# Optimization experiments

Measured on AMD Instinct MI355X. Metric: run time of the kernel, lower is better.

The kernel has to match this reference:

```python
import jax, jax.numpy as jnp
import numpy as np

D_MODEL = 1024
N_HEADS = 16
D_HEAD = 64
B, S = 8, 1024
EPS = 1.1920929e-07  # torch.finfo(float32).eps, RMSNorm default eps=None


def setup_inputs() -> dict:
    key = jax.random.key(0)
    k1, k2, k3 = jax.random.split(key, 3)
    x = jax.random.normal(k1, (B, S, D_MODEL), dtype=jnp.float32)
    W_qkv = jax.random.normal(k2, (3 * N_HEADS * D_HEAD, D_MODEL), dtype=jnp.float32) * 0.02
    b_qkv = jnp.zeros((3 * N_HEADS * D_HEAD,), dtype=jnp.float32)
    W_o = jax.random.normal(k3, (D_MODEL, N_HEADS * D_HEAD), dtype=jnp.float32) * 0.02
    b_o = jnp.zeros((D_MODEL,), dtype=jnp.float32)
    return {"x": x, "W_qkv": W_qkv, "b_qkv": b_qkv, "W_o": W_o, "b_o": b_o}


def reference(x, W_qkv, b_qkv, W_o, b_o):
    # RMSNorm, no affine
    normed = x * jax.lax.rsqrt(jnp.mean(x * x, axis=-1, keepdims=True) + EPS)
    qkv = normed @ W_qkv.T + b_qkv                       # [b, s, 3*H*Dh]
    # packing order '(n_heads d_head n_qkv)' -> reshape (H, Dh, 3), unbind last
    qkv = qkv.reshape(*qkv.shape[:-1], N_HEADS, D_HEAD, 3)
    q, k, v = qkv[..., 0], qkv[..., 1], qkv[..., 2]       # [b, s, H, Dh]
    scores = jnp.einsum('bqhd,bkhd->bhqk', q, k)          # no 1/sqrt(d) scaling
    seq = x.shape[-2]
    causal_mask = jnp.triu(jnp.ones((seq, seq), dtype=bool), k=1)  # True above diag
    scores = jnp.where(causal_mask, -jnp.inf, scores)
    # NOTE: softmax over the QUERY axis (dim=-2), faithful to the source
    attn = jax.nn.softmax(scores, axis=-2)                # [b, h, q, k]
    z = jnp.einsum('bhqk,bkhd->bqhd', attn, v)            # [b, q, H, Dh]
    z = z.reshape(*z.shape[:-2], N_HEADS * D_HEAD)
    return z @ W_o.T + b_o
```

## Files before the change

### kernel.cpp

```cpp
#include <hip/hip_runtime.h>
#include <hip/hip_bf16.h>

typedef _Float16 f16;
typedef _Float16 f16x8 __attribute__((ext_vector_type(8)));
typedef _Float16 f16x4 __attribute__((ext_vector_type(4)));
typedef float f32x4 __attribute__((ext_vector_type(4)));

constexpr int Bb = 8, Ss = 1024, Hh = 16, DH = 64, DM = 1024, N3 = 3072;
constexpr int Mm = Bb * Ss;
constexpr float EPS = 1.1920929e-07f;

__device__ __forceinline__ void gll16(const f16* g, f16* l) {
    __builtin_amdgcn_global_load_lds(
        (__attribute__((address_space(1))) void*)(g),
        (__attribute__((address_space(3))) void*)(l), 16, 0, 0);
}

__global__ void prep_kernel(const float* __restrict__ x, f16* __restrict__ xh,
                            const float* __restrict__ Wqkv, const float* __restrict__ Wo,
                            f16* __restrict__ wq, f16* __restrict__ wo) {
    const int t = threadIdx.x;
    const int blk = blockIdx.x;
    if (blk < Mm) {
        const int row = blk;
        float4 v = *(const float4*)(x + (size_t)row * DM + t * 4);
        float s = v.x * v.x + v.y * v.y + v.z * v.z + v.w * v.w;
#pragma unroll
        for (int o = 32; o > 0; o >>= 1) s += __shfl_down(s, o, 64);
        __shared__ float red[4];
        if ((t & 63) == 0) red[t >> 6] = s;
        __syncthreads();
        float tot = red[0] + red[1] + red[2] + red[3];
        float sc = rsqrtf(tot * (1.0f / DM) + EPS);
        f16x4 hv = {(f16)(v.x * sc), (f16)(v.y * sc), (f16)(v.z * sc), (f16)(v.w * sc)};
        *(f16x4*)(xh + (size_t)row * DM + t * 4) = hv;
    } else if (blk < Mm + N3) {
        int j = blk - Mm;
        int h = j / 192, r = j % 192, d = r / 3, wh = r % 3;
        int rp = wh * 1024 + h * 64 + d;
        float4 v = *(const float4*)(Wqkv + (size_t)j * DM + t * 4);
        f16x4 hv = {(f16)v.x, (f16)v.y, (f16)v.z, (f16)v.w};
        *(f16x4*)(wq + (size_t)rp * DM + t * 4) = hv;
    } else {
        int j = blk - Mm - N3;
        float4 v = *(const float4*)(Wo + (size_t)j * DM + t * 4);
        f16x4 hv = {(f16)v.x, (f16)v.y, (f16)v.z, (f16)v.w};
        *(f16x4*)(wo + (size_t)j * DM + t * 4) = hv;
    }
}

__launch_bounds__(256, 2)
__global__ void qkv_gemm(const f16* __restrict__ xh, const f16* __restrict__ wq,
                         const float* __restrict__ bqkv, f16* __restrict__ qk,
                         f16* __restrict__ vT) {
    __shared__ __align__(16) f16 smem[17536];
    f16* As = smem;
    f16* Bs = smem + 8192;
    f16* Cs = smem;
    const int t = threadIdx.x, lane = t & 63, w = t >> 6;
    const int bid = blockIdx.y * gridDim.x + blockIdx.x;
    const int swz = (bid & 7) * 192 + (bid >> 3);
    const int gm0 = (swz / 24) * 128, gn0 = (swz % 24) * 128;
    const int wm = (w >> 1) * 64, wn = (w & 1) * 64;
    const int srow = lane >> 3, sslot = (lane & 7) ^ srow;
    const int r15 = lane & 15, cs = lane >> 4;

    const f16* Ag = xh + (size_t)(gm0 + srow) * DM + sslot * 8;
    const f16* Bg = wq + (size_t)(gn0 + srow) * DM + sslot * 8;

    int aoff[4][2], boff[4][2];
#pragma unroll
    for (int i = 0; i < 4; ++i) {
        int Ra = wm + i * 16 + r15;
        aoff[i][0] = Ra * 64 + ((cs ^ (Ra & 7)) * 8);
        aoff[i][1] = Ra * 64 + (((cs + 4) ^ (Ra & 7)) * 8);
        int Rb = wn + i * 16 + r15;
        boff[i][0] = Rb * 64 + ((cs ^ (Rb & 7)) * 8);
        boff[i][1] = Rb * 64 + (((cs + 4) ^ (Rb & 7)) * 8);
    }
    f32x4 acc[4][4] = {};

    for (int k0 = 0; k0 < DM; k0 += 64) {
        __syncthreads();
#pragma unroll
        for (int j = 0; j < 4; ++j) {
            int c = w * 4 + j;
            gll16(Ag + (size_t)c * 8 * DM + k0, As + c * 512);
            gll16(Bg + (size_t)c * 8 * DM + k0, Bs + c * 512);
        }
        __syncthreads();
#pragma unroll
        for (int half = 0; half < 2; ++half) {
            f16x8 af[4], bf[4];
#pragma unroll
            for (int i = 0; i < 4; ++i) af[i] = *(const f16x8*)&As[aoff[i][half]];
#pragma unroll
            for (int i = 0; i < 4; ++i) bf[i] = *(const f16x8*)&Bs[boff[i][half]];
#pragma unroll
            for (int mi = 0; mi < 4; ++mi)
#pragma unroll
                for (int ni = 0; ni < 4; ++ni)
                    acc[mi][ni] = __builtin_amdgcn_mfma_f32_16x16x32_f16(af[mi], bf[ni], acc[mi][ni], 0, 0, 0);
        }
    }

    const int which = gn0 >> 10;
    const int CSTR = (which == 2) ? 137 : 136;
    __syncthreads();
#pragma unroll
    for (int ni = 0; ni < 4; ++ni) {
        int jcolp = gn0 + wn + ni * 16 + r15;
        int rr = jcolp & 1023, hh = rr >> 6, dd = rr & 63;
        float bb = bqkv[hh * 192 + dd * 3 + which];
#pragma unroll
        for (int mi = 0; mi < 4; ++mi)
#pragma unroll
            for (int jj = 0; jj < 4; ++jj)
                Cs[(wm + mi * 16 + cs * 4 + jj) * CSTR + (wn + ni * 16 + r15)] =
                    (f16)(acc[mi][ni][jj] + bb);
    }
    __syncthreads();
    const int bglob = gm0 >> 10;
    const int sbase = gm0 & 1023;
    if (which < 2) {
        f16* dstb = qk + (size_t)which * (Bb * Hh) * (Ss * DH);
#pragma unroll
        for (int it = 0; it < 8; ++it) {
            int lin = it * 2048 + t * 8;
            int row = lin >> 7, c0 = lin & 127;
            f16x8 v = *(const f16x8*)&Cs[row * 136 + c0];
            int rr = (gn0 + c0) & 1023;
            int hh = rr >> 6, d0 = rr & 63;
            *(f16x8*)(dstb + ((size_t)(bglob * Hh + hh)) * (Ss * DH) +
                      (size_t)(sbase + row) * DH + d0) = v;
        }
    } else {
#pragma unroll
        for (int it = 0; it < 8; ++it) {
            int col = it * 16 + (t >> 4);
            int s0 = (t & 15) * 8;
            f16x8 v;
#pragma unroll
            for (int e = 0; e < 8; ++e) v[e] = Cs[(s0 + e) * 137 + col];
            int rr = (gn0 + col) & 1023;
            int hh = rr >> 6, dd = rr & 63;
            *(f16x8*)(vT + ((size_t)(bglob * Hh + hh) * DH + dd) * Ss + sbase + s0) = v;
        }
    }
}

__launch_bounds__(512, 2)
__global__ void colstats_kernel(const f16* __restrict__ qk, float* __restrict__ cbuf) {
    __shared__ __align__(16) f16 Qs[2][128 * 64];
    const int t = threadIdx.x, lane = t & 63, w = t >> 6;
    const int r15 = lane & 15, cs = lane >> 4;
    const int srow = lane >> 3, sslot = (lane & 7) ^ srow;
    const int bh = blockIdx.y, si = blockIdx.x;
    const int kA0 = si * 128, kB0 = (7 - si) * 128;
    const size_t hs = (size_t)(Bb * Hh) * (Ss * DH);
    const f16* qb = qk + (size_t)bh * (Ss * DH);
    const f16* kb = qb + hs;

    const int kwA = kA0 + w * 16, kglobA = kwA + r15;
    const int kwB = kB0 + w * 16, kglobB = kwB + r15;
    f16x8 kfA0 = *(const f16x8*)(kb + (size_t)(kwA + r15) * DH + cs * 8);
    f16x8 kfA1 = *(const f16x8*)(kb + (size_t)(kwA + r15) * DH + 32 + cs * 8);
    f16x8 kfB0 = *(const f16x8*)(kb + (size_t)(kwB + r15) * DH + cs * 8);
    f16x8 kfB1 = *(const f16x8*)(kb + (size_t)(kwB + r15) * DH + 32 + cs * 8);

    gll16(qb + (size_t)(si * 128 + w * 16 + srow) * DH + sslot * 8, Qs[0] + (2 * w) * 512);
    gll16(qb + (size_t)(si * 128 + w * 16 + 8 + srow) * DH + sslot * 8, Qs[0] + (2 * w + 1) * 512);
    __syncthreads();
    float la = 0.0f, lb = 0.0f;
    int cur = 0;

    for (int qt2 = si; qt2 < 8; ++qt2) {
        if (qt2 + 1 < 8) {
            gll16(qb + (size_t)((qt2 + 1) * 128 + w * 16 + srow) * DH + sslot * 8,
                  Qs[cur ^ 1] + (2 * w) * 512);
            gll16(qb + (size_t)((qt2 + 1) * 128 + w * 16 + 8 + srow) * DH + sslot * 8,
                  Qs[cur ^ 1] + (2 * w + 1) * 512);
        }
#pragma unroll
        for (int qs = 0; qs < 8; ++qs) {
            const int qb16 = qt2 * 128 + qs * 16;
            const bool nA = (qb16 + 15 >= kwA);
            const bool nB = (qb16 + 15 >= kwB);
            if (!(nA || nB)) continue;
            int Ra = qs * 16 + r15;
            f16x8 a0 = *(const f16x8*)&Qs[cur][Ra * 64 + ((cs ^ (Ra & 7)) * 8)];
            f16x8 a1 = *(const f16x8*)&Qs[cur][Ra * 64 + (((cs + 4) ^ (Ra & 7)) * 8)];
            if (nA) {
                f32x4 sf = {};
                sf = __builtin_amdgcn_mfma_f32_16x16x32_f16(a0, kfA0, sf, 0, 0, 0);
                sf = __builtin_amdgcn_mfma_f32_16x16x32_f16(a1, kfA1, sf, 0, 0, 0);
#pragma unroll
                for (int j = 0; j < 4; ++j) {
                    int q = qb16 + cs * 4 + j;
                    la += (q >= kglobA) ? __expf(sf[j]) : 0.0f;
                }
            }
            if (nB) {
                f32x4 sf = {};
                sf = __builtin_amdgcn_mfma_f32_16x16x32_f16(a0, kfB0, sf, 0, 0, 0);
                sf = __builtin_amdgcn_mfma_f32_16x16x32_f16(a1, kfB1, sf, 0, 0, 0);
#pragma unroll
                for (int j = 0; j < 4; ++j) {
                    int q = qb16 + cs * 4 + j;
                    lb += (q >= kglobB) ? __expf(sf[j]) : 0.0f;
                }
            }
        }
        __syncthreads();
        cur ^= 1;
    }
    la += __shfl_xor(la, 16, 64);
    la += __shfl_xor(la, 32, 64);
    lb += __shfl_xor(lb, 16, 64);
    lb += __shfl_xor(lb, 32, 64);
    if (cs == 0) {
        cbuf[bh * Ss + kglobA] = logf(la);
        cbuf[bh * Ss + kglobB] = logf(lb);
    }
}

__launch_bounds__(512, 2)
__global__ void attnz_kernel(const f16* __restrict__ qk, const f16* __restrict__ vT,
                             const float* __restrict__ cbuf, f16* __restrict__ z) {
    __shared__ __align__(16) f16 Ks[64 * 64];
    __shared__ __align__(16) f16 Vs[64 * 64];
    __shared__ __align__(16) float cb[1024];
    const int t = threadIdx.x, lane = t & 63, w = t >> 6;
    const int r15 = lane & 15, cs = lane >> 4;
    const int srow = lane >> 3, sslot = (lane & 7) ^ srow;
    const int bh = blockIdx.y, si = blockIdx.x;
    const int qtA = si, qtB = 7 - si;
    const size_t hs = (size_t)(Bb * Hh) * (Ss * DH);
    const f16* qb = qk + (size_t)bh * (Ss * DH);
    const f16* kb = qb + hs;
    const f16* vb = vT + (size_t)bh * (DH * Ss);

    const int qwA = qtA * 128 + w * 16, qA = qwA + r15;
    const int qwB = qtB * 128 + w * 16, qB = qwB + r15;
    f16x8 aqA0 = *(const f16x8*)(qb + (size_t)(qwA + r15) * DH + cs * 8);
    f16x8 aqA1 = *(const f16x8*)(qb + (size_t)(qwA + r15) * DH + 32 + cs * 8);
    f16x8 aqB0 = *(const f16x8*)(qb + (size_t)(qwB + r15) * DH + cs * 8);
    f16x8 aqB1 = *(const f16x8*)(qb + (size_t)(qwB + r15) * DH + 32 + cs * 8);

    gll16(kb + (size_t)(w * 8 + srow) * DH + sslot * 8, Ks + w * 512);
    gll16(vb + (size_t)(w * 8 + srow) * Ss + sslot * 8, Vs + w * 512);
    {
        float2 c2 = *(const float2*)(cbuf + bh * Ss + t * 2);
        *(float2*)&cb[t * 2] = c2;
    }
    __syncthreads();
    f32x4 accA[4] = {}, accB[4] = {};
    const int nktA = 2 * qtA + 2, nktB = 2 * qtB + 2;
    const int sAl = ((cs & 1) * 2) * 16 + r15;
    const int sBl = sAl + 16;
    const bool hi = (cs >> 1) != 0;

    for (int kt = 0; kt < nktB; ++kt) {
        if (kt) {
            __syncthreads();
            gll16(kb + (size_t)(kt * 64 + w * 8 + srow) * DH + sslot * 8, Ks + w * 512);
            gll16(vb + (size_t)(w * 8 + srow) * Ss + kt * 64 + sslot * 8, Vs + w * 512);
            __syncthreads();
        }
        const int kb0 = kt * 64;
        const bool doA = (kt < nktA) && (kb0 <= qwA + 15);
        const bool doB = (kb0 <= qwB + 15);
        if (!(doA || doB)) continue;

        unsigned pkA[4][2], pkB[4][2];
#pragma unroll
        for (int tl = 0; tl < 4; ++tl) {
            const int kbase = kb0 + tl * 16;
            const bool nA = doA && (kbase <= qwA + 15);
            const bool nB = doB && (kbase <= qwB + 15);
            pkA[tl][0] = 0u; pkA[tl][1] = 0u;
            pkB[tl][0] = 0u; pkB[tl][1] = 0u;
            if (!(nA || nB)) continue;
            int Rk2 = tl * 16 + r15;
            f16x8 kf0 = *(const f16x8*)&Ks[Rk2 * 64 + ((cs ^ (Rk2 & 7)) * 8)];
            f16x8 kf1 = *(const f16x8*)&Ks[Rk2 * 64 + (((cs + 4) ^ (Rk2 & 7)) * 8)];
            f32x4 cv = *(const f32x4*)&cb[kbase + cs * 4];
            if (nA) {
                f32x4 sf = {};
                sf = __builtin_amdgcn_mfma_f32_16x16x32_f16(kf0, aqA0, sf, 0, 0, 0);
                sf = __builtin_amdgcn_mfma_f32_16x16x32_f16(kf1, aqA1, sf, 0, 0, 0);
                f16 p[4];
#pragma unroll
                for (int j = 0; j < 4; ++j) {
                    int k = kbase + cs * 4 + j;
                    p[j] = (f16)((k <= qA) ? __expf(sf[j] - cv[j]) : 0.0f);
                }
                union { f16 h[2]; unsigned u; } u0, u1;
                u0.h[0] = p[0]; u0.h[1] = p[1];
                u1.h[0] = p[2]; u1.h[1] = p[3];
                pkA[tl][0] = u0.u; pkA[tl][1] = u1.u;
            }
            if (nB) {
                f32x4 sf = {};
                sf = __builtin_amdgcn_mfma_f32_16x16x32_f16(kf0, aqB0, sf, 0, 0, 0);
                sf = __builtin_amdgcn_mfma_f32_16x16x32_f16(kf1, aqB1, sf, 0, 0, 0);
                f16 p[4];
#pragma unroll
                for (int j = 0; j < 4; ++j) {
                    int k = kbase + cs * 4 + j;
                    p[j] = (f16)((k <= qB) ? __expf(sf[j] - cv[j]) : 0.0f);
                }
                union { f16 h[2]; unsigned u; } u0, u1;
                u0.h[0] = p[0]; u0.h[1] = p[1];
                u1.h[0] = p[2]; u1.h[1] = p[3];
                pkB[tl][0] = u0.u; pkB[tl][1] = u1.u;
            }
        }
        f16x8 bfA[2], bfB[2];
        bool uA[2], uB[2];
#pragma unroll
        for (int c = 0; c < 2; ++c) {
            uA[c] = doA && (kb0 + c * 32 <= qwA + 15);
            uB[c] = doB && (kb0 + c * 32 <= qwB + 15);
            if (uA[c]) {
                unsigned a0 = (unsigned)__shfl((int)pkA[2 * c][0], sAl, 64);
                unsigned a1 = (unsigned)__shfl((int)pkA[2 * c][1], sAl, 64);
                unsigned a2 = (unsigned)__shfl((int)pkA[2 * c][0], sBl, 64);
                unsigned a3 = (unsigned)__shfl((int)pkA[2 * c][1], sBl, 64);
                unsigned b0_ = (unsigned)__shfl((int)pkA[2 * c + 1][0], sAl, 64);
                unsigned b1_ = (unsigned)__shfl((int)pkA[2 * c + 1][1], sAl, 64);
                unsigned b2_ = (unsigned)__shfl((int)pkA[2 * c + 1][0], sBl, 64);
                unsigned b3_ = (unsigned)__shfl((int)pkA[2 * c + 1][1], sBl, 64);
                union { unsigned u[4]; f16x8 v; } bf;
                bf.u[0] = hi ? b0_ : a0;
                bf.u[1] = hi ? b1_ : a1;
                bf.u[2] = hi ? b2_ : a2;
                bf.u[3] = hi ? b3_ : a3;
                bfA[c] = bf.v;
            }
            if (uB[c]) {
                unsigned a0 = (unsigned)__shfl((int)pkB[2 * c][0], sAl, 64);
                unsigned a1 = (unsigned)__shfl((int)pkB[2 * c][1], sAl, 64);
                unsigned a2 = (unsigned)__shfl((int)pkB[2 * c][0], sBl, 64);
                unsigned a3 = (unsigned)__shfl((int)pkB[2 * c][1], sBl, 64);
                unsigned b0_ = (unsigned)__shfl((int)pkB[2 * c + 1][0], sAl, 64);
                unsigned b1_ = (unsigned)__shfl((int)pkB[2 * c + 1][1], sAl, 64);
                unsigned b2_ = (unsigned)__shfl((int)pkB[2 * c + 1][0], sBl, 64);
                unsigned b3_ = (unsigned)__shfl((int)pkB[2 * c + 1][1], sBl, 64);
                union { unsigned u[4]; f16x8 v; } bf;
                bf.u[0] = hi ? b0_ : a0;
                bf.u[1] = hi ? b1_ : a1;
                bf.u[2] = hi ? b2_ : a2;
                bf.u[3] = hi ? b3_ : a3;
                bfB[c] = bf.v;
            }
        }
#pragma unroll
        for (int dt = 0; dt < 4; ++dt) {
            int Rv = dt * 16 + r15;
            f16x8 v0 = *(const f16x8*)&Vs[Rv * 64 + ((cs ^ (Rv & 7)) * 8)];
            f16x8 v1 = *(const f16x8*)&Vs[Rv * 64 + (((4 + cs) ^ (Rv & 7)) * 8)];
            if (uA[0]) accA[dt] = __builtin_amdgcn_mfma_f32_16x16x32_f16(v0, bfA[0], accA[dt], 0, 0, 0);
            if (uA[1]) accA[dt] = __builtin_amdgcn_mfma_f32_16x16x32_f16(v1, bfA[1], accA[dt], 0, 0, 0);
            if (uB[0]) accB[dt] = __builtin_amdgcn_mfma_f32_16x16x32_f16(v0, bfB[0], accB[dt], 0, 0, 0);
            if (uB[1]) accB[dt] = __builtin_amdgcn_mfma_f32_16x16x32_f16(v1, bfB[1], accB[dt], 0, 0, 0);
        }
    }
    const int b = bh >> 4, h = bh & 15;
#pragma unroll
    for (int dt = 0; dt < 4; ++dt) {
        f16x4 zvA = {(f16)accA[dt][0], (f16)accA[dt][1], (f16)accA[dt][2], (f16)accA[dt][3]};
        *(f16x4*)(z + ((size_t)(b * Ss + qA)) * DM + h * DH + dt * 16 + cs * 4) = zvA;
        f16x4 zvB = {(f16)accB[dt][0], (f16)accB[dt][1], (f16)accB[dt][2], (f16)accB[dt][3]};
        *(f16x4*)(z + ((size_t)(b * Ss + qB)) * DM + h * DH + dt * 16 + cs * 4) = zvB;
    }
}

__launch_bounds__(256, 2)
__global__ void out_gemm(const f16* __restrict__ z, const f16* __restrict__ wo,
                         const float* __restrict__ bo, float* __restrict__ out) {
    __shared__ __align__(16) char smem[128 * 132 * 4];
    f16* As = (f16*)smem;
    f16* Bs = (f16*)(smem + 16384);
    float* Cs = (float*)smem;
    const int t = threadIdx.x, lane = t & 63, w = t >> 6;
    const int bid = blockIdx.y * gridDim.x + blockIdx.x;
    const int swz = (bid & 7) * 64 + (bid >> 3);
    const int gm0 = (swz / 8) * 128, gn0 = (swz % 8) * 128;
    const int wm = (w >> 1) * 64, wn = (w & 1) * 64;
    const int srow = lane >> 3, sslot = (lane & 7) ^ srow;
    const int r15 = lane & 15, cs = lane >> 4;

    const f16* Ag = z + (size_t)(gm0 + srow) * DM + sslot * 8;
    const f16* Bg = wo + (size_t)(gn0 + srow) * DM + sslot * 8;

    int aoff[4][2], boff[4][2];
#pragma unroll
    for (int i = 0; i < 4; ++i) {
        int Ra = wm + i * 16 + r15;
        aoff[i][0] = Ra * 64 + ((cs ^ (Ra & 7)) * 8);
        aoff[i][1] = Ra * 64 + (((cs + 4) ^ (Ra & 7)) * 8);
        int Rb = wn + i * 16 + r15;
        boff[i][0] = Rb * 64 + ((cs ^ (Rb & 7)) * 8);
        boff[i][1] = Rb * 64 + (((cs + 4) ^ (Rb & 7)) * 8);
    }
    f32x4 acc[4][4] = {};

    for (int k0 = 0; k0 < DM; k0 += 64) {
        __syncthreads();
#pragma unroll
        for (int j = 0; j < 4; ++j) {
            int c = w * 4 + j;
            gll16(Ag + (size_t)c * 8 * DM + k0, As + c * 512);
            gll16(Bg + (size_t)c * 8 * DM + k0, Bs + c * 512);
        }
        __syncthreads();
#pragma unroll
        for (int half = 0; half < 2; ++half) {
            f16x8 af[4], bf[4];
#pragma unroll
            for (int i = 0; i < 4; ++i) af[i] = *(const f16x8*)&As[aoff[i][half]];
#pragma unroll
            for (int i = 0; i < 4; ++i) bf[i] = *(const f16x8*)&Bs[boff[i][half]];
#pragma unroll
            for (int mi = 0; mi < 4; ++mi)
#pragma unroll
                for (int ni = 0; ni < 4; ++ni)
                    acc[mi][ni] = __builtin_amdgcn_mfma_f32_16x16x32_f16(af[mi], bf[ni], acc[mi][ni], 0, 0, 0);
        }
    }
    __syncthreads();
#pragma unroll
    for (int ni = 0; ni < 4; ++ni) {
        float bb = bo[gn0 + wn + ni * 16 + r15];
#pragma unroll
        for (int mi = 0; mi < 4; ++mi)
#pragma unroll
            for (int jj = 0; jj < 4; ++jj)
                Cs[(wm + mi * 16 + cs * 4 + jj) * 132 + (wn + ni * 16 + r15)] =
                    acc[mi][ni][jj] + bb;
    }
    __syncthreads();
#pragma unroll
    for (int it = 0; it < 16; ++it) {
        int idx = it * 256 + t;
        int row = idx >> 5, c0 = (idx & 31) * 4;
        float4 v = *(const float4*)&Cs[row * 132 + c0];
        *(float4*)(out + (size_t)(gm0 + row) * DM + gn0 + c0) = v;
    }
}

extern "C" void kernel_launch(void* const* d_in, const int* in_sizes, int n_in,
                              void* d_out, int out_size, void* d_ws, size_t ws_size,
                              hipStream_t stream) {
    (void)in_sizes; (void)n_in; (void)out_size; (void)ws_size;
    const float* x    = (const float*)d_in[0];
    const float* Wqkv = (const float*)d_in[1];
    const float* bqkv = (const float*)d_in[2];
    const float* Wo   = (const float*)d_in[3];
    const float* bo   = (const float*)d_in[4];
    float* out = (float*)d_out;

    char* ws = (char*)d_ws;
    f16* xh   = (f16*)ws;
    f16* z    = (f16*)ws;
    f16* wq   = (f16*)(ws + 16777216);
    f16* wo   = (f16*)(ws + 23068672);
    f16* qk   = (f16*)(ws + 25165824);
    f16* vT   = (f16*)(ws + 58720256);
    float* cbuf = (float*)(ws + 75497472);

    prep_kernel<<<Mm + N3 + DM, 256, 0, stream>>>(x, xh, Wqkv, Wo, wq, wo);
    qkv_gemm<<<dim3(N3 / 128, Mm / 128), 256, 0, stream>>>(xh, wq, bqkv, qk, vT);
    colstats_kernel<<<dim3(4, Bb * Hh), 512, 0, stream>>>(qk, cbuf);
    attnz_kernel<<<dim3(4, Bb * Hh), 512, 0, stream>>>(qk, vT, cbuf, z);
    out_gemm<<<dim3(DM / 128, Mm / 128), 256, 0, stream>>>(z, wo, bo, out);
}
```

Baseline: 177.3 us.

## Double K/V tile depth in attention and raise launch-bounds occupancy hint

The attention-Z kernel now stages 128 keys of K and V per iteration instead of 64, halving the number of barrier-separated load phases. The V tile uses a wider 128-column layout with a 16-way XOR swizzle. Both colstats and attnz get a launch-bounds minimum of 8 blocks per CU instead of 2, which caps register use per thread. The cost is more LDS per block, a coarser causal tail that may load a useless half tile, and possible register spilling under the tighter bound.

```diff
diff --git a/kernel.cpp b/kernel.cpp
--- a/kernel.cpp
+++ b/kernel.cpp
@@ -149,7 +149,7 @@
     }
 }
 
-__launch_bounds__(512, 2)
+__launch_bounds__(512, 8)
 __global__ void colstats_kernel(const f16* __restrict__ qk, float* __restrict__ cbuf) {
     __shared__ __align__(16) f16 Qs[2][128 * 64];
     const int t = threadIdx.x, lane = t & 63, w = t >> 6;
@@ -224,15 +224,16 @@
     }
 }
 
-__launch_bounds__(512, 2)
+__launch_bounds__(512, 8)
 __global__ void attnz_kernel(const f16* __restrict__ qk, const f16* __restrict__ vT,
                              const float* __restrict__ cbuf, f16* __restrict__ z) {
-    __shared__ __align__(16) f16 Ks[64 * 64];
-    __shared__ __align__(16) f16 Vs[64 * 64];
+    __shared__ __align__(16) f16 Ks[128 * 64];
+    __shared__ __align__(16) f16 Vs[64 * 128];
     __shared__ __align__(16) float cb[1024];
     const int t = threadIdx.x, lane = t & 63, w = t >> 6;
     const int r15 = lane & 15, cs = lane >> 4;
     const int srow = lane >> 3, sslot = (lane & 7) ^ srow;
+    const int vrow = lane >> 4, vg = lane & 15;
     const int bh = blockIdx.y, si = blockIdx.x;
     const int qtA = si, qtB = 7 - si;
     const size_t hs = (size_t)(Bb * Hh) * (Ss * DH);
@@ -247,123 +248,136 @@
     f16x8 aqB0 = *(const f16x8*)(qb + (size_t)(qwB + r15) * DH + cs * 8);
     f16x8 aqB1 = *(const f16x8*)(qb + (size_t)(qwB + r15) * DH + 32 + cs * 8);
 
-    gll16(kb + (size_t)(w * 8 + srow) * DH + sslot * 8, Ks + w * 512);
-    gll16(vb + (size_t)(w * 8 + srow) * Ss + sslot * 8, Vs + w * 512);
+#pragma unroll
+    for (int j = 0; j < 2; ++j) {
+        int c = 2 * w + j;
+        gll16(kb + (size_t)(8 * c + srow) * DH + sslot * 8, Ks + c * 512);
+        int rv = 4 * c + vrow;
+        gll16(vb + (size_t)rv * Ss + (vg ^ (rv & 15)) * 8, Vs + c * 512);
+    }
     {
         float2 c2 = *(const float2*)(cbuf + bh * Ss + t * 2);
         *(float2*)&cb[t * 2] = c2;
     }
     __syncthreads();
     f32x4 accA[4] = {}, accB[4] = {};
-    const int nktA = 2 * qtA + 2, nktB = 2 * qtB + 2;
+    const int nkt2 = qtB + 1;
     const int sAl = ((cs & 1) * 2) * 16 + r15;
     const int sBl = sAl + 16;
     const bool hi = (cs >> 1) != 0;
 
-    for (int kt = 0; kt < nktB; ++kt) {
-        if (kt) {
+    for (int kt2 = 0; kt2 < nkt2; ++kt2) {
+        if (kt2) {
             __syncthreads();
-            gll16(kb + (size_t)(kt * 64 + w * 8 + srow) * DH + sslot * 8, Ks + w * 512);
-            gll16(vb + (size_t)(w * 8 + srow) * Ss + kt * 64 + sslot * 8, Vs + w * 512);
+#pragma unroll
+            for (int j = 0; j < 2; ++j) {
+                int c = 2 * w + j;
+                gll16(kb + (size_t)(kt2 * 128 + 8 * c + srow) * DH + sslot * 8, Ks + c * 512);
+                int rv = 4 * c + vrow;
+                gll16(vb + (size_t)rv * Ss + kt2 * 128 + (vg ^ (rv & 15)) * 8, Vs + c * 512);
+            }
             __syncthreads();
         }
-        const int kb0 = kt * 64;
-        const bool doA = (kt < nktA) && (kb0 <= qwA + 15);
-        const bool doB = (kb0 <= qwB + 15);
-        if (!(doA || doB)) continue;
-
-        unsigned pkA[4][2], pkB[4][2];
-#pragma unroll
-        for (int tl = 0; tl < 4; ++tl) {
-            const int kbase = kb0 + tl * 16;
-            const bool nA = doA && (kbase <= qwA + 15);
-            const bool nB = doB && (kbase <= qwB + 15);
-            pkA[tl][0] = 0u; pkA[tl][1] = 0u;
-            pkB[tl][0] = 0u; pkB[tl][1] = 0u;
-            if (!(nA || nB)) continue;
-            int Rk2 = tl * 16 + r15;
-            f16x8 kf0 = *(const f16x8*)&Ks[Rk2 * 64 + ((cs ^ (Rk2 & 7)) * 8)];
-            f16x8 kf1 = *(const f16x8*)&Ks[Rk2 * 64 + (((cs + 4) ^ (Rk2 & 7)) * 8)];
-            f32x4 cv = *(const f32x4*)&cb[kbase + cs * 4];
-            if (nA) {
-                f32x4 sf = {};
-                sf = __builtin_amdgcn_mfma_f32_16x16x32_f16(kf0, aqA0, sf, 0, 0, 0);
-                sf = __builtin_amdgcn_mfma_f32_16x16x32_f16(kf1, aqA1, sf, 0, 0, 0);
-                f16 p[4];
-#pragma unroll
-                for (int j = 0; j < 4; ++j) {
-                    int k = kbase + cs * 4 + j;
-                    p[j] = (f16)((k <= qA) ? __expf(sf[j] - cv[j]) : 0.0f);
-                }
-                union { f16 h[2]; unsigned u; } u0, u1;
-                u0.h[0] = p[0]; u0.h[1] = p[1];
-                u1.h[0] = p[2]; u1.h[1] = p[3];
-                pkA[tl][0] = u0.u; pkA[tl][1] = u1.u;
-            }
-            if (nB) {
-                f32x4 sf = {};
-                sf = __builtin_amdgcn_mfma_f32_16x16x32_f16(kf0, aqB0, sf, 0, 0, 0);
-                sf = __builtin_amdgcn_mfma_f32_16x16x32_f16(kf1, aqB1, sf, 0, 0, 0);
-                f16 p[4];
-#pragma unroll
-                for (int j = 0; j < 4; ++j) {
-                    int k = kbase + cs * 4 + j;
-                    p[j] = (f16)((k <= qB) ? __expf(sf[j] - cv[j]) : 0.0f);
-                }
-                union { f16 h[2]; unsigned u; } u0, u1;
-                u0.h[0] = p[0]; u0.h[1] = p[1];
-                u1.h[0] = p[2]; u1.h[1] = p[3];
-                pkB[tl][0] = u0.u; pkB[tl][1] = u1.u;
-            }
-        }
-        f16x8 bfA[2], bfB[2];
-        bool uA[2], uB[2];
-#pragma unroll
-        for (int c = 0; c < 2; ++c) {
-            uA[c] = doA && (kb0 + c * 32 <= qwA + 15);
-            uB[c] = doB && (kb0 + c * 32 <= qwB + 15);
-            if (uA[c]) {
-                unsigned a0 = (unsigned)__shfl((int)pkA[2 * c][0], sAl, 64);
-                unsigned a1 = (unsigned)__shfl((int)pkA[2 * c][1], sAl, 64);
-                unsigned a2 = (unsigned)__shfl((int)pkA[2 * c][0], sBl, 64);
-                unsigned a3 = (unsigned)__shfl((int)pkA[2 * c][1], sBl, 64);
-                unsigned b0_ = (unsigned)__shfl((int)pkA[2 * c + 1][0], sAl, 64);
-                unsigned b1_ = (unsigned)__shfl((int)pkA[2 * c + 1][1], sAl, 64);
-                unsigned b2_ = (unsigned)__shfl((int)pkA[2 * c + 1][0], sBl, 64);
-                unsigned b3_ = (unsigned)__shfl((int)pkA[2 * c + 1][1], sBl, 64);
-                union { unsigned u[4]; f16x8 v; } bf;
-                bf.u[0] = hi ? b0_ : a0;
-                bf.u[1] = hi ? b1_ : a1;
-                bf.u[2] = hi ? b2_ : a2;
-                bf.u[3] = hi ? b3_ : a3;
-                bfA[c] = bf.v;
-            }
-            if (uB[c]) {
-                unsigned a0 = (unsigned)__shfl((int)pkB[2 * c][0], sAl, 64);
-                unsigned a1 = (unsigned)__shfl((int)pkB[2 * c][1], sAl, 64);
-                unsigned a2 = (unsigned)__shfl((int)pkB[2 * c][0], sBl, 64);
-                unsigned a3 = (unsigned)__shfl((int)pkB[2 * c][1], sBl, 64);
-                unsigned b0_ = (unsigned)__shfl((int)pkB[2 * c + 1][0], sAl, 64);
-                unsigned b1_ = (unsigned)__shfl((int)pkB[2 * c + 1][1], sAl, 64);
-                unsigned b2_ = (unsigned)__shfl((int)pkB[2 * c + 1][0], sBl, 64);
-                unsigned b3_ = (unsigned)__shfl((int)pkB[2 * c + 1][1], sBl, 64);
-                union { unsigned u[4]; f16x8 v; } bf;
-                bf.u[0] = hi ? b0_ : a0;
-                bf.u[1] = hi ? b1_ : a1;
-                bf.u[2] = hi ? b2_ : a2;
-                bf.u[3] = hi ? b3_ : a3;
-                bfB[c] = bf.v;
-            }
-        }
-#pragma unroll
-        for (int dt = 0; dt < 4; ++dt) {
-            int Rv = dt * 16 + r15;
-            f16x8 v0 = *(const f16x8*)&Vs[Rv * 64 + ((cs ^ (Rv & 7)) * 8)];
-            f16x8 v1 = *(const f16x8*)&Vs[Rv * 64 + (((4 + cs) ^ (Rv & 7)) * 8)];
-            if (uA[0]) accA[dt] = __builtin_amdgcn_mfma_f32_16x16x32_f16(v0, bfA[0], accA[dt], 0, 0, 0);
-            if (uA[1]) accA[dt] = __builtin_amdgcn_mfma_f32_16x16x32_f16(v1, bfA[1], accA[dt], 0, 0, 0);
-            if (uB[0]) accB[dt] = __builtin_amdgcn_mfma_f32_16x16x32_f16(v0, bfB[0], accB[dt], 0, 0, 0);
-            if (uB[1]) accB[dt] = __builtin_amdgcn_mfma_f32_16x16x32_f16(v1, bfB[1], accB[dt], 0, 0, 0);
+#pragma unroll
+        for (int ht = 0; ht < 2; ++ht) {
+            const int kb0 = kt2 * 128 + ht * 64;
+            const bool doA = (kb0 <= qwA + 15);
+            const bool doB = (kb0 <= qwB + 15);
+            if (!(doA || doB)) continue;
+
+            unsigned pkA[4][2], pkB[4][2];
+#pragma unroll
+            for (int tl = 0; tl < 4; ++tl) {
+                const int kbase = kb0 + tl * 16;
+                const bool nA = doA && (kbase <= qwA + 15);
+                const bool nB = doB && (kbase <= qwB + 15);
+                pkA[tl][0] = 0u; pkA[tl][1] = 0u;
+                pkB[tl][0] = 0u; pkB[tl][1] = 0u;
+                if (!(nA || nB)) continue;
+                int Rk2 = ht * 64 + tl * 16 + r15;
+                f16x8 kf0 = *(const f16x8*)&Ks[Rk2 * 64 + ((cs ^ (Rk2 & 7)) * 8)];
+                f16x8 kf1 = *(const f16x8*)&Ks[Rk2 * 64 + (((cs + 4) ^ (Rk2 & 7)) * 8)];
+                f32x4 cv = *(const f32x4*)&cb[kbase + cs * 4];
+                if (nA) {
+                    f32x4 sf = {};
+                    sf = __builtin_amdgcn_mfma_f32_16x16x32_f16(kf0, aqA0, sf, 0, 0, 0);
+                    sf = __builtin_amdgcn_mfma_f32_16x16x32_f16(kf1, aqA1, sf, 0, 0, 0);
+                    f16 p[4];
+#pragma unroll
+                    for (int j = 0; j < 4; ++j) {
+                        int k = kbase + cs * 4 + j;
+                        p[j] = (f16)((k <= qA) ? __expf(sf[j] - cv[j]) : 0.0f);
+                    }
+                    union { f16 h[2]; unsigned u; } u0, u1;
+                    u0.h[0] = p[0]; u0.h[1] = p[1];
+                    u1.h[0] = p[2]; u1.h[1] = p[3];
+                    pkA[tl][0] = u0.u; pkA[tl][1] = u1.u;
+                }
+                if (nB) {
+                    f32x4 sf = {};
+                    sf = __builtin_amdgcn_mfma_f32_16x16x32_f16(kf0, aqB0, sf, 0, 0, 0);
+                    sf = __builtin_amdgcn_mfma_f32_16x16x32_f16(kf1, aqB1, sf, 0, 0, 0);
+                    f16 p[4];
+#pragma unroll
+                    for (int j = 0; j < 4; ++j) {
+                        int k = kbase + cs * 4 + j;
+                        p[j] = (f16)((k <= qB) ? __expf(sf[j] - cv[j]) : 0.0f);
+                    }
+                    union { f16 h[2]; unsigned u; } u0, u1;
+                    u0.h[0] = p[0]; u0.h[1] = p[1];
+                    u1.h[0] = p[2]; u1.h[1] = p[3];
+                    pkB[tl][0] = u0.u; pkB[tl][1] = u1.u;
+                }
+            }
+            f16x8 bfA[2], bfB[2];
+            bool uA[2], uB[2];
+#pragma unroll
+            for (int c = 0; c < 2; ++c) {
+                uA[c] = doA && (kb0 + c * 32 <= qwA + 15);
+                uB[c] = doB && (kb0 + c * 32 <= qwB + 15);
+                if (uA[c]) {
+                    unsigned a0 = (unsigned)__shfl((int)pkA[2 * c][0], sAl, 64);
+                    unsigned a1 = (unsigned)__shfl((int)pkA[2 * c][1], sAl, 64);
+                    unsigned a2 = (unsigned)__shfl((int)pkA[2 * c][0], sBl, 64);
+                    unsigned a3 = (unsigned)__shfl((int)pkA[2 * c][1], sBl, 64);
+                    unsigned b0_ = (unsigned)__shfl((int)pkA[2 * c + 1][0], sAl, 64);
+                    unsigned b1_ = (unsigned)__shfl((int)pkA[2 * c + 1][1], sAl, 64);
+                    unsigned b2_ = (unsigned)__shfl((int)pkA[2 * c + 1][0], sBl, 64);
+                    unsigned b3_ = (unsigned)__shfl((int)pkA[2 * c + 1][1], sBl, 64);
+                    union { unsigned u[4]; f16x8 v; } bf;
+                    bf.u[0] = hi ? b0_ : a0;
+                    bf.u[1] = hi ? b1_ : a1;
+                    bf.u[2] = hi ? b2_ : a2;
+                    bf.u[3] = hi ? b3_ : a3;
+                    bfA[c] = bf.v;
+                }
+                if (uB[c]) {
+                    unsigned a0 = (unsigned)__shfl((int)pkB[2 * c][0], sAl, 64);
+                    unsigned a1 = (unsigned)__shfl((int)pkB[2 * c][1], sAl, 64);
+                    unsigned a2 = (unsigned)__shfl((int)pkB[2 * c][0], sBl, 64);
+                    unsigned a3 = (unsigned)__shfl((int)pkB[2 * c][1], sBl, 64);
+                    unsigned b0_ = (unsigned)__shfl((int)pkB[2 * c + 1][0], sAl, 64);
+                    unsigned b1_ = (unsigned)__shfl((int)pkB[2 * c + 1][1], sAl, 64);
+                    unsigned b2_ = (unsigned)__shfl((int)pkB[2 * c + 1][0], sBl, 64);
+                    unsigned b3_ = (unsigned)__shfl((int)pkB[2 * c + 1][1], sBl, 64);
+                    union { unsigned u[4]; f16x8 v; } bf;
+                    bf.u[0] = hi ? b0_ : a0;
+                    bf.u[1] = hi ? b1_ : a1;
+                    bf.u[2] = hi ? b2_ : a2;
+                    bf.u[3] = hi ? b3_ : a3;
+                    bfB[c] = bf.v;
+                }
+            }
+#pragma unroll
+            for (int dt = 0; dt < 4; ++dt) {
+                int Rv = dt * 16 + r15;
+                f16x8 v0 = *(const f16x8*)&Vs[Rv * 128 + (((ht * 8 + cs) ^ (Rv & 15)) * 8)];
+                f16x8 v1 = *(const f16x8*)&Vs[Rv * 128 + (((ht * 8 + 4 + cs) ^ (Rv & 15)) * 8)];
+                if (uA[0]) accA[dt] = __builtin_amdgcn_mfma_f32_16x16x32_f16(v0, bfA[0], accA[dt], 0, 0, 0);
+                if (uA[1]) accA[dt] = __builtin_amdgcn_mfma_f32_16x16x32_f16(v1, bfA[1], accA[dt], 0, 0, 0);
+                if (uB[0]) accB[dt] = __builtin_amdgcn_mfma_f32_16x16x32_f16(v0, bfB[0], accB[dt], 0, 0, 0);
+                if (uB[1]) accB[dt] = __builtin_amdgcn_mfma_f32_16x16x32_f16(v1, bfB[1], accB[dt], 0, 0, 0);
+            }
         }
     }
     const int b = bh >> 4, h = bh & 15;
```

Result: slower. 367.7 us (+107.4%).
